# Kernel tuning notes

Measured on AMD Instinct MI355X. Metric: run time of the kernel, lower is better.

The kernel has to match this reference:

```python
import jax, jax.numpy as jnp
import numpy as np
import math

B, S, L, K, NSTEPS = 32, 128, 4096, 129, 10
PAD = K // 2  # torch: int(kernel.shape[-1]/2)


def _grouped_xcorr(x, w):
    # torch F.conv1d semantics (cross-correlation), groups = channels
    # x: [B,C,L] f32, w: [C,1,K] f32 -> [B,C,L]
    return jax.lax.conv_general_dilated(
        x, w, window_strides=(1,), padding=[(PAD, PAD)],
        dimension_numbers=('NCH', 'OIH', 'NCH'), feature_group_count=x.shape[1])


def _matched_filter(x_re, x_im, k_re, k_im):
    # complex grouped conv with conj(kernel) repeated per pulse
    wc_re = jnp.tile(k_re[None, None, :], (S, 1, 1))
    wc_im = jnp.tile(-k_im[None, None, :], (S, 1, 1))  # conj
    out_re = _grouped_xcorr(x_re, wc_re) - _grouped_xcorr(x_im, wc_im)
    out_im = _grouped_xcorr(x_re, wc_im) + _grouped_xcorr(x_im, wc_re)
    return out_re + 1j * out_im  # complex64 [B,S,L]


def _produce_rd(x, w_mag, w_phase):
    phase = jnp.arctan(w_phase)                    # [B,S]
    norm_mag = S * jax.nn.softmax(w_mag, axis=-1)  # [B,S]
    iq = (norm_mag * jnp.exp(-1j * phase))[..., None] * x
    return jnp.fft.fftshift(jnp.fft.fft(iq, axis=-2), axes=-2)


def _circular_weighted_mean(w):
    # circular weighted mean of index over last axis; returns (magnitude, index)
    N = w.shape[-1]
    ang = (2.0 * jnp.pi / N) * jnp.arange(N, dtype=w.dtype)
    z = jnp.sum(w * jnp.exp(1j * ang), axis=-1)
    return jnp.abs(z), jnp.angle(z) / (2.0 * jnp.pi) * N


def _snr(rd):
    Bn, nfft, Ln = rd.shape
    e = jnp.abs(rd) ** 2                                   # [B,S,L]
    flat_idx = jnp.argmax(e.reshape(Bn, -1), axis=1)
    max_range = flat_idx % Ln                              # [B] (indices: constant wrt grad)
    col = jnp.take_along_axis(e, max_range[:, None, None], axis=2)[..., 0]  # [B,S]
    _, peak_idx = _circular_weighted_mean(col)
    # torch rounds + casts to int -> detached index
    idx = jax.lax.stop_gradient(jnp.round(peak_idx)).astype(jnp.int32) % nfft
    peak = jnp.take_along_axis(col, idx[:, None], axis=1)[:, 0]
    noise = (jnp.sum(col, axis=-1) - peak) / (nfft - 1)
    return 10.0 * jnp.log10(peak) - 10.0 * jnp.log10(noise)


def setup_inputs() -> dict:
    key = jax.random.key(0)
    ks = jax.random.split(key, 5)
    return {
        'x_re': jax.random.normal(ks[0], (B, S, L), jnp.float32),
        'x_im': jax.random.normal(ks[1], (B, S, L), jnp.float32),
        'kernel_re': jax.random.normal(ks[2], (K,), jnp.float32),
        'kernel_im': jax.random.normal(ks[3], (K,), jnp.float32),
        'log_step_mag': -2.0 * jnp.ones((S, NSTEPS), jnp.float32),
        'log_step_phase': -2.0 * jnp.ones((S, NSTEPS), jnp.float32),
        'w_phase_init': jax.random.uniform(ks[4], (B, S), jnp.float32),
    }


def reference(x_re, x_im, kernel_re, kernel_im, log_step_mag, log_step_phase, w_phase_init):
    x = _matched_filter(x_re, x_im, kernel_re, kernel_im)  # [B,S,L] complex64
    w_mag = jnp.ones((B, S), jnp.float32)
    w_phase = w_phase_init

    def loss_sum(wm, wp):
        return jnp.sum(_snr(_produce_rd(x, wm, wp)))

    grad_fn = jax.grad(loss_sum, argnums=(0, 1))
    ln10 = math.log(10.0)
    for i in range(NSTEPS):
        # torch detaches w_mag/w_phase before the inner autograd.grad
        g_mag, g_phase = grad_fn(jax.lax.stop_gradient(w_mag),
                                 jax.lax.stop_gradient(w_phase))
        lr_mag = jnp.exp(log_step_mag[:, i] * ln10)    # 10**log_step
        lr_phase = jnp.exp(log_step_phase[:, i] * ln10)
        w_mag = w_mag + lr_mag * g_mag
        w_phase = w_phase + lr_phase * g_phase
    return jnp.mean(_snr(_produce_rd(x, w_mag, w_phase)))
```

## Files before the change

### kernel.cpp

```cpp
#include <hip/hip_runtime.h>

#define BB 32
#define SS 128
#define LL 4096
#define KK 129
#define NST 10

constexpr double PI_D = 3.141592653589793238462643383279502884;
constexpr double red_sin(double x){
  double x2 = x*x, t = x, r = x;
  t *= -x2/6.0;   r += t;
  t *= -x2/20.0;  r += t;
  t *= -x2/42.0;  r += t;
  t *= -x2/72.0;  r += t;
  t *= -x2/110.0; r += t;
  t *= -x2/156.0; r += t;
  t *= -x2/210.0; r += t;
  t *= -x2/272.0; r += t;
  return r;
}
constexpr double csin_d(double x){
  while (x >  PI_D) x -= 2.0*PI_D;
  while (x < -PI_D) x += 2.0*PI_D;
  if (x >  PI_D*0.5)      x =  PI_D - x;
  else if (x < -PI_D*0.5) x = -PI_D - x;
  return red_sin(x);
}
constexpr double ccos_d(double x){ return csin_d(x + PI_D*0.5); }
struct TWT { float c[64]; float s[64]; };
constexpr TWT make_tw(){
  TWT t{};
  for (int j = 0; j < 64; j++){
    double a = -2.0*PI_D*(double)j/128.0;
    t.c[j] = (float)ccos_d(a);
    t.s[j] = (float)csin_d(a);
  }
  return t;
}
constexpr TWT TW = make_tw();

__global__ __launch_bounds__(256) void mf_kernel(const float* __restrict__ xr,
                                                 const float* __restrict__ xi,
                                                 const float* __restrict__ kr,
                                                 const float* __restrict__ ki,
                                                 float2* __restrict__ out)
{
  const int row = blockIdx.x;
  const int t = threadIdx.x;
  __shared__ float2 xs[LL + KK - 1];
  __shared__ float2 ks[KK];
  const float* xrr = xr + (size_t)row*LL;
  const float* xir = xi + (size_t)row*LL;
  for (int i = t; i < LL + KK - 1; i += 256){
    int l = i - 64;
    float a = (l >= 0 && l < LL) ? xrr[l] : 0.0f;
    float c = (l >= 0 && l < LL) ? xir[l] : 0.0f;
    xs[i] = make_float2(a, c);
  }
  if (t < KK) ks[t] = make_float2(kr[t], ki[t]);
  __syncthreads();

  float2 acc[16];
  #pragma unroll
  for (int j = 0; j < 16; j++) acc[j] = make_float2(0.0f, 0.0f);

  for (int k = 0; k < KK; k++){
    const float2 w = ks[k];
    #pragma unroll
    for (int j = 0; j < 16; j++){
      float2 xv = xs[t + j*256 + k];
      acc[j].x += xv.x*w.x + xv.y*w.y;
      acc[j].y += xv.y*w.x - xv.x*w.y;
    }
  }
  float2* orow = out + (size_t)row*LL;
  #pragma unroll
  for (int j = 0; j < 16; j++) orow[t + j*256] = acc[j];
}

__global__ void init_kernel(const float* __restrict__ wpi,
                            float* __restrict__ w_mag, float* __restrict__ w_phase,
                            float2* __restrict__ cvec, unsigned long long* __restrict__ slots,
                            float* __restrict__ out)
{
  const int i = blockIdx.x*256 + threadIdx.x;
  if (i < BB*SS){
    float wp = wpi[i];
    w_mag[i] = 1.0f;
    w_phase[i] = wp;
    float phi = atanf(wp);
    float s, c;
    sincosf(phi, &s, &c);
    cvec[i] = make_float2(c, -s);
  }
  if (i < BB) slots[i] = 0ull;
  if (i == 0) out[0] = 0.0f;
}

template<int SPAN>
__device__ __forceinline__ void fstage(float2* v){
  #pragma unroll
  for (int base = 0; base < 64; base += 2*SPAN){
    #pragma unroll
    for (int j = 0; j < SPAN; j++){
      const int i0 = base + j, i1 = base + j + SPAN;
      float ax = v[i0].x, ay = v[i0].y, bx = v[i1].x, by = v[i1].y;
      float sx = ax - bx, sy = ay - by;
      v[i0].x = ax + bx; v[i0].y = ay + by;
      const int tj = j * (64 / SPAN);
      if (tj == 0){
        v[i1].x = sx; v[i1].y = sy;
      } else if (tj == 32){
        v[i1].x = sy; v[i1].y = -sx;
      } else {
        const float wr = TW.c[tj], wi = TW.s[tj];
        v[i1].x = sx*wr - sy*wi;
        v[i1].y = sy*wr + sx*wi;
      }
    }
  }
}

__global__ __launch_bounds__(256) void scan_kernel(const float2* __restrict__ xmf,
                                                   const float2* __restrict__ cvec,
                                                   unsigned long long* __restrict__ slots)
{
  const int b = blockIdx.y;
  const int tid = threadIdx.x;
  const int p = tid >> 1, r = tid & 1;
  const int l = blockIdx.x*128 + p;
  __shared__ float2 csh[SS];
  __shared__ unsigned long long red[256];
  if (tid < SS) csh[tid] = cvec[b*SS + tid];
  __syncthreads();

  const float2* xb = xmf + ((size_t)(b*SS + r*64))*LL + l;
  float2 v[64];
  #pragma unroll
  for (int j = 0; j < 64; j++){
    float2 x = xb[(size_t)j*LL];
    float2 c = csh[r*64 + j];
    v[j].x = c.x*x.x - c.y*x.y;
    v[j].y = c.x*x.y + c.y*x.x;
  }
  const float sgn = r ? -1.0f : 1.0f;
  #pragma unroll
  for (int j = 0; j < 64; j++){
    float px = __shfl_xor(v[j].x, 1);
    float py = __shfl_xor(v[j].y, 1);
    float ux = fmaf(sgn, v[j].x, px);
    float uy = fmaf(sgn, v[j].y, py);
    float wr = r ? TW.c[j] : 1.0f;
    float wi = r ? TW.s[j] : 0.0f;
    v[j].x = ux*wr - uy*wi;
    v[j].y = uy*wr + ux*wi;
  }
  fstage<32>(v); fstage<16>(v); fstage<8>(v);
  fstage<4>(v);  fstage<2>(v);  fstage<1>(v);

  float mm = 0.0f;
  #pragma unroll
  for (int j = 0; j < 64; j++) mm = fmaxf(mm, v[j].x*v[j].x + v[j].y*v[j].y);
  mm = fmaxf(mm, __shfl_xor(mm, 1));

  unsigned long long pk = ((unsigned long long)__float_as_uint(mm) << 32) | (unsigned int)l;
  red[tid] = pk;
  __syncthreads();
  #pragma unroll
  for (int st = 128; st > 0; st >>= 1){
    if (tid < st){ unsigned long long o = red[tid + st]; if (o > red[tid]) red[tid] = o; }
    __syncthreads();
  }
  if (tid == 0) atomicMax(slots + b, red[0]);
}

__device__ __forceinline__ float bsum(float v, float* red, int t){
  __syncthreads();
  red[t] = v; __syncthreads();
  #pragma unroll
  for (int st = 64; st > 0; st >>= 1){
    if (t < st) red[t] += red[t + st];
    __syncthreads();
  }
  return red[0];
}
__device__ __forceinline__ float bmax(float v, float* red, int t){
  __syncthreads();
  red[t] = v; __syncthreads();
  #pragma unroll
  for (int st = 64; st > 0; st >>= 1){
    if (t < st) red[t] = fmaxf(red[t], red[t + st]);
    __syncthreads();
  }
  return red[0];
}

__global__ __launch_bounds__(128) void step_kernel(const float2* __restrict__ xmf,
                                                   float* __restrict__ w_mag,
                                                   float* __restrict__ w_phase,
                                                   float2* __restrict__ cvec,
                                                   unsigned long long* __restrict__ slots,
                                                   const float* __restrict__ lsm,
                                                   const float* __restrict__ lsp,
                                                   int stepi, int isFinal,
                                                   float* __restrict__ out)
{
  const int b = blockIdx.x, t = threadIdx.x;
  __shared__ float red[128];
  __shared__ float2 ysh[128];
  __shared__ float twc[128], tws[128];
  __shared__ float speak;
  __shared__ int sidx;

  const int rbin = (int)(slots[b] & 0xffffffffull);
  float wm = w_mag[b*SS + t];
  float wp = w_phase[b*SS + t];
  const float2 xc = xmf[((size_t)(b*SS + t))*LL + rbin];
  float phi = atanf(wp);
  float sph, cph;
  sincosf(phi, &sph, &cph);
  {
    float sv, cv;
    sincosf((float)(2.0*PI_D/128.0) * (float)t, &sv, &cv);
    twc[t] = cv; tws[t] = -sv;
  }
  float mx = bmax(wm, red, t);
  float ex = expf(wm - mx);
  float sm = bsum(ex, red, t);
  float m = 128.0f * ex / sm;
  float cre = m*cph, cim = -m*sph;
  ysh[t] = make_float2(cre*xc.x - cim*xc.y, cre*xc.y + cim*xc.x);
  __syncthreads();

  float Fr = 0.0f, Fi = 0.0f;
  #pragma unroll 8
  for (int s2 = 0; s2 < 128; s2++){
    int id = (t*s2) & 127;
    float wr = twc[id], wi = tws[id];
    float2 ys = ysh[s2];
    Fr += wr*ys.x - wi*ys.y;
    Fi += wr*ys.y + wi*ys.x;
  }
  const int u = (t + 64) & 127;
  float colu = Fr*Fr + Fi*Fi;

  float total = bsum(colu, red, t);
  float zre = bsum(colu * twc[u], red, t);
  float zim = bsum(colu * (-tws[u]), red, t);
  if (t == 0){
    float ang = atan2f(zim, zre);
    float pidx = ang * (128.0f/(2.0f*(float)PI_D));
    float rr = rintf(pidx);
    sidx = ((int)rr) & 127;
  }
  __syncthreads();
  const int idx = sidx;
  if (u == idx) speak = colu;
  __syncthreads();
  const float peak = speak;
  const float noise = (total - peak) * (1.0f/127.0f);

  if (isFinal){
    if (t == 0) atomicAdd(out, 10.0f*(log10f(peak) - log10f(noise)) * (1.0f/(float)BB));
    return;
  }

  constexpr float C10 = 4.342944819032518f;
  float g = (u == idx) ? (C10/peak) : (-C10/(127.0f*noise));
  __syncthreads();
  ysh[t] = make_float2(2.0f*g*Fr, 2.0f*g*Fi);
  __syncthreads();

  float Tr = 0.0f, Ti = 0.0f;
  #pragma unroll 8
  for (int k = 0; k < 128; k++){
    int id = (t*k) & 127;
    float wr = twc[id], wi = -tws[id];
    float2 G = ysh[k];
    Tr += wr*G.x - wi*G.y;
    Ti += wr*G.y + wi*G.x;
  }
  float Hr = xc.x*Tr + xc.y*Ti;
  float Hi = xc.x*Ti - xc.y*Tr;
  float dm   = Hr*cph - Hi*sph;
  float dphi = -m*(Hr*sph + Hi*cph);
  float S1 = bsum(m*dm, red, t);
  float gwm = m*(dm - S1*(1.0f/128.0f));
  float gwp = dphi / (1.0f + wp*wp);

  constexpr float LN10 = 2.302585092994046f;
  float lrm = expf(lsm[t*NST + stepi] * LN10);
  float lrp = expf(lsp[t*NST + stepi] * LN10);
  wm += lrm*gwm;
  wp += lrp*gwp;
  w_mag[b*SS + t] = wm;
  w_phase[b*SS + t] = wp;

  float mx2 = bmax(wm, red, t);
  float ex2 = expf(wm - mx2);
  float sm2 = bsum(ex2, red, t);
  float m2 = 128.0f * ex2 / sm2;
  float phi2 = atanf(wp);
  float s2v, c2v;
  sincosf(phi2, &s2v, &c2v);
  cvec[b*SS + t] = make_float2(m2*c2v, -m2*s2v);
  if (t == 0) slots[b] = 0ull;
}

extern "C" void kernel_launch(void* const* d_in, const int* in_sizes, int n_in,
                              void* d_out, int out_size, void* d_ws, size_t ws_size,
                              hipStream_t stream)
{
  const float* x_re = (const float*)d_in[0];
  const float* x_im = (const float*)d_in[1];
  const float* k_re = (const float*)d_in[2];
  const float* k_im = (const float*)d_in[3];
  const float* lsm  = (const float*)d_in[4];
  const float* lsp  = (const float*)d_in[5];
  const float* wpi  = (const float*)d_in[6];
  float* out = (float*)d_out;

  char* ws = (char*)d_ws;
  size_t off = 0;
  float2* xmf = (float2*)(ws + off);                 off += (size_t)BB*SS*LL*sizeof(float2);
  unsigned long long* slots = (unsigned long long*)(ws + off); off += 256;
  float* w_mag   = (float*)(ws + off);               off += (size_t)BB*SS*4;
  float* w_phase = (float*)(ws + off);               off += (size_t)BB*SS*4;
  float2* cvec   = (float2*)(ws + off);              off += (size_t)BB*SS*8;
  if (ws_size < off) return;

  mf_kernel<<<BB*SS, 256, 0, stream>>>(x_re, x_im, k_re, k_im, xmf);
  init_kernel<<<(BB*SS + 255)/256, 256, 0, stream>>>(wpi, w_mag, w_phase, cvec, slots, out);
  for (int i = 0; i < NST; i++){
    scan_kernel<<<dim3(LL/128, BB), 256, 0, stream>>>(xmf, cvec, slots);
    step_kernel<<<BB, 128, 0, stream>>>(xmf, w_mag, w_phase, cvec, slots, lsm, lsp, i, 0, out);
  }
  scan_kernel<<<dim3(LL/128, BB), 256, 0, stream>>>(xmf, cvec, slots);
  step_kernel<<<BB, 128, 0, stream>>>(xmf, w_mag, w_phase, cvec, slots, lsm, lsp, 0, 1, out);
}
```

Measured before the change: 917.8 us.

## Register-window matched filter, 4-way split FFT scan, wave-shuffle reductions in step kernel

```diff
diff --git a/kernel.cpp b/kernel.cpp
--- a/kernel.cpp
+++ b/kernel.cpp
@@ -39,6 +39,8 @@
 }
 constexpr TWT TW = make_tw();
 
+#define PHYS(i) ((i) + (((i) >> 4) << 1))
+
 __global__ __launch_bounds__(256) void mf_kernel(const float* __restrict__ xr,
                                                  const float* __restrict__ xi,
                                                  const float* __restrict__ kr,
@@ -47,7 +49,7 @@
 {
   const int row = blockIdx.x;
   const int t = threadIdx.x;
-  __shared__ float2 xs[LL + KK - 1];
+  __shared__ float2 xs[4752];
   __shared__ float2 ks[KK];
   const float* xrr = xr + (size_t)row*LL;
   const float* xir = xi + (size_t)row*LL;
@@ -55,27 +57,62 @@
     int l = i - 64;
     float a = (l >= 0 && l < LL) ? xrr[l] : 0.0f;
     float c = (l >= 0 && l < LL) ? xir[l] : 0.0f;
-    xs[i] = make_float2(a, c);
+    xs[PHYS(i)] = make_float2(a, c);
   }
   if (t < KK) ks[t] = make_float2(kr[t], ki[t]);
   __syncthreads();
 
+  const int base = t*16;
   float2 acc[16];
   #pragma unroll
   for (int j = 0; j < 16; j++) acc[j] = make_float2(0.0f, 0.0f);
 
-  for (int k = 0; k < KK; k++){
-    const float2 w = ks[k];
+  float2 win[32];
+  #pragma unroll
+  for (int i = 0; i < 32; i++) win[i] = xs[PHYS(base + i)];
+
+  #pragma unroll 1
+  for (int kb2 = 0; kb2 < 4; ++kb2){
     #pragma unroll
-    for (int j = 0; j < 16; j++){
-      float2 xv = xs[t + j*256 + k];
-      acc[j].x += xv.x*w.x + xv.y*w.y;
-      acc[j].y += xv.y*w.x - xv.x*w.y;
+    for (int half = 0; half < 2; ++half){
+      #pragma unroll
+      for (int kk = 0; kk < 16; ++kk){
+        const float2 w = ks[kb2*32 + half*16 + kk];
+        #pragma unroll
+        for (int j = 0; j < 16; ++j){
+          const float2 xv = win[(half*16 + kk + j) & 31];
+          acc[j].x = fmaf(xv.x, w.x, acc[j].x);
+          acc[j].x = fmaf(xv.y, w.y, acc[j].x);
+          acc[j].y = fmaf(xv.y, w.x, acc[j].y);
+          acc[j].y = fmaf(-xv.x, w.y, acc[j].y);
+        }
+      }
+      if (kb2 < 3 || half == 0){
+        const int vb = kb2*32 + half*16 + 32;
+        #pragma unroll
+        for (int i = 0; i < 16; ++i){
+          win[half*16 + i] = xs[PHYS(base + vb + i)];
+        }
+      }
     }
   }
-  float2* orow = out + (size_t)row*LL;
-  #pragma unroll
-  for (int j = 0; j < 16; j++) orow[t + j*256] = acc[j];
+  {
+    const float2 w = ks[128];
+    #pragma unroll
+    for (int j = 0; j < 16; ++j){
+      const float2 xv = win[j];
+      acc[j].x = fmaf(xv.x, w.x, acc[j].x);
+      acc[j].x = fmaf(xv.y, w.y, acc[j].x);
+      acc[j].y = fmaf(xv.y, w.x, acc[j].y);
+      acc[j].y = fmaf(-xv.x, w.y, acc[j].y);
+    }
+  }
+
+  float4* orow = (float4*)(out + (size_t)row*LL + base);
+  #pragma unroll
+  for (int q = 0; q < 8; ++q){
+    orow[q] = make_float4(acc[2*q].x, acc[2*q].y, acc[2*q+1].x, acc[2*q+1].y);
+  }
 }
 
 __global__ void init_kernel(const float* __restrict__ wpi,
@@ -97,13 +134,13 @@
   if (i == 0) out[0] = 0.0f;
 }
 
-template<int SPAN>
+template<int SPAN, int N>
 __device__ __forceinline__ void fstage(float2* v){
   #pragma unroll
-  for (int base = 0; base < 64; base += 2*SPAN){
+  for (int b0 = 0; b0 < N; b0 += 2*SPAN){
     #pragma unroll
     for (int j = 0; j < SPAN; j++){
-      const int i0 = base + j, i1 = base + j + SPAN;
+      const int i0 = b0 + j, i1 = b0 + j + SPAN;
       float ax = v[i0].x, ay = v[i0].y, bx = v[i1].x, by = v[i1].y;
       float sx = ax - bx, sy = ay - by;
       v[i0].x = ax + bx; v[i0].y = ay + by;
@@ -127,75 +164,95 @@
 {
   const int b = blockIdx.y;
   const int tid = threadIdx.x;
-  const int p = tid >> 1, r = tid & 1;
-  const int l = blockIdx.x*128 + p;
+  const int f = tid >> 2, r = tid & 3;
+  const int l = blockIdx.x*64 + f;
   __shared__ float2 csh[SS];
-  __shared__ unsigned long long red[256];
   if (tid < SS) csh[tid] = cvec[b*SS + tid];
   __syncthreads();
 
-  const float2* xb = xmf + ((size_t)(b*SS + r*64))*LL + l;
-  float2 v[64];
-  #pragma unroll
-  for (int j = 0; j < 64; j++){
+  const float2* xb = xmf + ((size_t)(b*SS + r*32))*LL + l;
+  float2 v[32];
+  #pragma unroll
+  for (int j = 0; j < 32; ++j){
     float2 x = xb[(size_t)j*LL];
-    float2 c = csh[r*64 + j];
+    float2 c = csh[r*32 + j];
     v[j].x = c.x*x.x - c.y*x.y;
     v[j].y = c.x*x.y + c.y*x.x;
   }
-  const float sgn = r ? -1.0f : 1.0f;
-  #pragma unroll
-  for (int j = 0; j < 64; j++){
-    float px = __shfl_xor(v[j].x, 1);
-    float py = __shfl_xor(v[j].y, 1);
-    float ux = fmaf(sgn, v[j].x, px);
-    float uy = fmaf(sgn, v[j].y, py);
-    float wr = r ? TW.c[j] : 1.0f;
-    float wi = r ? TW.s[j] : 0.0f;
-    v[j].x = ux*wr - uy*wi;
-    v[j].y = uy*wr + ux*wi;
-  }
-  fstage<32>(v); fstage<16>(v); fstage<8>(v);
-  fstage<4>(v);  fstage<2>(v);  fstage<1>(v);
+  {
+    const bool hi = (r & 2) != 0;
+    const float sgn = hi ? -1.0f : 1.0f;
+    const bool odd = (r & 1) != 0;
+    #pragma unroll
+    for (int j = 0; j < 32; ++j){
+      float px = __shfl_xor(v[j].x, 2);
+      float py = __shfl_xor(v[j].y, 2);
+      float ux = fmaf(sgn, v[j].x, px);
+      float uy = fmaf(sgn, v[j].y, py);
+      float wr = hi ? (odd ? TW.s[j] : TW.c[j]) : 1.0f;
+      float wi = hi ? (odd ? -TW.c[j] : TW.s[j]) : 0.0f;
+      v[j].x = ux*wr - uy*wi;
+      v[j].y = uy*wr + ux*wi;
+    }
+  }
+  {
+    const bool hi = (r & 1) != 0;
+    const float sgn = hi ? -1.0f : 1.0f;
+    #pragma unroll
+    for (int j = 0; j < 32; ++j){
+      float px = __shfl_xor(v[j].x, 1);
+      float py = __shfl_xor(v[j].y, 1);
+      float ux = fmaf(sgn, v[j].x, px);
+      float uy = fmaf(sgn, v[j].y, py);
+      float wr = hi ? TW.c[2*j] : 1.0f;
+      float wi = hi ? TW.s[2*j] : 0.0f;
+      v[j].x = ux*wr - uy*wi;
+      v[j].y = uy*wr + ux*wi;
+    }
+  }
+  fstage<16,32>(v); fstage<8,32>(v); fstage<4,32>(v); fstage<2,32>(v); fstage<1,32>(v);
 
   float mm = 0.0f;
   #pragma unroll
-  for (int j = 0; j < 64; j++) mm = fmaxf(mm, v[j].x*v[j].x + v[j].y*v[j].y);
+  for (int j = 0; j < 32; ++j) mm = fmaxf(mm, v[j].x*v[j].x + v[j].y*v[j].y);
   mm = fmaxf(mm, __shfl_xor(mm, 1));
+  mm = fmaxf(mm, __shfl_xor(mm, 2));
 
   unsigned long long pk = ((unsigned long long)__float_as_uint(mm) << 32) | (unsigned int)l;
-  red[tid] = pk;
-  __syncthreads();
-  #pragma unroll
-  for (int st = 128; st > 0; st >>= 1){
-    if (tid < st){ unsigned long long o = red[tid + st]; if (o > red[tid]) red[tid] = o; }
-    __syncthreads();
-  }
-  if (tid == 0) atomicMax(slots + b, red[0]);
-}
-
-__device__ __forceinline__ float bsum(float v, float* red, int t){
-  __syncthreads();
-  red[t] = v; __syncthreads();
-  #pragma unroll
-  for (int st = 64; st > 0; st >>= 1){
-    if (t < st) red[t] += red[t + st];
-    __syncthreads();
-  }
-  return red[0];
-}
-__device__ __forceinline__ float bmax(float v, float* red, int t){
-  __syncthreads();
-  red[t] = v; __syncthreads();
-  #pragma unroll
-  for (int st = 64; st > 0; st >>= 1){
-    if (t < st) red[t] = fmaxf(red[t], red[t + st]);
-    __syncthreads();
-  }
-  return red[0];
-}
-
-__global__ __launch_bounds__(128) void step_kernel(const float2* __restrict__ xmf,
+  #pragma unroll
+  for (int m = 4; m < 64; m <<= 1){
+    unsigned long long o = __shfl_xor(pk, m);
+    if (o > pk) pk = o;
+  }
+  if ((tid & 63) == 0) atomicMax(slots + b, pk);
+}
+
+__device__ __forceinline__ float wredsum(float v){
+  #pragma unroll
+  for (int m = 1; m < 64; m <<= 1) v += __shfl_xor(v, m);
+  return v;
+}
+__device__ __forceinline__ float wredmax(float v){
+  #pragma unroll
+  for (int m = 1; m < 64; m <<= 1) v = fmaxf(v, __shfl_xor(v, m));
+  return v;
+}
+__device__ __forceinline__ float bsum256(float v, float* red4, int t){
+  v = wredsum(v);
+  __syncthreads();
+  if ((t & 63) == 0) red4[t >> 6] = v;
+  __syncthreads();
+  return red4[0] + red4[1] + red4[2] + red4[3];
+}
+__device__ __forceinline__ float bmax256(float v, float* red4, int t){
+  v = wredmax(v);
+  __syncthreads();
+  if ((t & 63) == 0) red4[t >> 6] = v;
+  __syncthreads();
+  return fmaxf(fmaxf(red4[0], red4[1]), fmaxf(red4[2], red4[3]));
+}
+
+__global__ __launch_bounds__(256) void step_kernel(const float2* __restrict__ xmf,
                                                    float* __restrict__ w_mag,
                                                    float* __restrict__ w_phase,
                                                    float2* __restrict__ cvec,
@@ -206,56 +263,61 @@
                                                    float* __restrict__ out)
 {
   const int b = blockIdx.x, t = threadIdx.x;
-  __shared__ float red[128];
-  __shared__ float2 ysh[128];
-  __shared__ float twc[128], tws[128];
+  const int s = t >> 1, h = t & 1;
+  __shared__ float2 ysh[SS];
+  __shared__ float twc[SS], tws[SS];
+  __shared__ float red4[4];
   __shared__ float speak;
   __shared__ int sidx;
 
   const int rbin = (int)(slots[b] & 0xffffffffull);
-  float wm = w_mag[b*SS + t];
-  float wp = w_phase[b*SS + t];
-  const float2 xc = xmf[((size_t)(b*SS + t))*LL + rbin];
-  float phi = atanf(wp);
+  const float wm0 = w_mag[b*SS + s];
+  const float wp0 = w_phase[b*SS + s];
+  const float2 xc = xmf[((size_t)(b*SS + s))*LL + rbin];
+  float phi = atanf(wp0);
   float sph, cph;
   sincosf(phi, &sph, &cph);
   {
+    int id = t & 127;
     float sv, cv;
-    sincosf((float)(2.0*PI_D/128.0) * (float)t, &sv, &cv);
-    twc[t] = cv; tws[t] = -sv;
-  }
-  float mx = bmax(wm, red, t);
-  float ex = expf(wm - mx);
-  float sm = bsum(ex, red, t);
+    sincosf((float)(2.0*PI_D/128.0) * (float)id, &sv, &cv);
+    twc[id] = cv; tws[id] = -sv;
+  }
+  float mx = bmax256(wm0, red4, t);
+  float ex = expf(wm0 - mx);
+  float sm = bsum256(ex, red4, t) * 0.5f;
   float m = 128.0f * ex / sm;
   float cre = m*cph, cim = -m*sph;
-  ysh[t] = make_float2(cre*xc.x - cim*xc.y, cre*xc.y + cim*xc.x);
-  __syncthreads();
-
+  ysh[s] = make_float2(cre*xc.x - cim*xc.y, cre*xc.y + cim*xc.x);
+  __syncthreads();
+
+  const int k = s;
   float Fr = 0.0f, Fi = 0.0f;
   #pragma unroll 8
-  for (int s2 = 0; s2 < 128; s2++){
-    int id = (t*s2) & 127;
+  for (int q = 0; q < 64; ++q){
+    int s2 = h*64 + q;
+    int id = (k*s2) & 127;
     float wr = twc[id], wi = tws[id];
     float2 ys = ysh[s2];
     Fr += wr*ys.x - wi*ys.y;
     Fi += wr*ys.y + wi*ys.x;
   }
-  const int u = (t + 64) & 127;
+  Fr += __shfl_xor(Fr, 1);
+  Fi += __shfl_xor(Fi, 1);
+  const int u = (k + 64) & 127;
   float colu = Fr*Fr + Fi*Fi;
 
-  float total = bsum(colu, red, t);
-  float zre = bsum(colu * twc[u], red, t);
-  float zim = bsum(colu * (-tws[u]), red, t);
+  float total = bsum256(colu, red4, t) * 0.5f;
+  float zre = bsum256(colu * twc[u], red4, t) * 0.5f;
+  float zim = bsum256(colu * (-tws[u]), red4, t) * 0.5f;
   if (t == 0){
     float ang = atan2f(zim, zre);
     float pidx = ang * (128.0f/(2.0f*(float)PI_D));
-    float rr = rintf(pidx);
-    sidx = ((int)rr) & 127;
+    sidx = ((int)rintf(pidx)) & 127;
   }
   __syncthreads();
   const int idx = sidx;
-  if (u == idx) speak = colu;
+  if (u == idx && h == 0) speak = colu;
   __syncthreads();
   const float peak = speak;
   const float noise = (total - peak) * (1.0f/127.0f);
@@ -268,42 +330,48 @@
   constexpr float C10 = 4.342944819032518f;
   float g = (u == idx) ? (C10/peak) : (-C10/(127.0f*noise));
   __syncthreads();
-  ysh[t] = make_float2(2.0f*g*Fr, 2.0f*g*Fi);
+  ysh[k] = make_float2(2.0f*g*Fr, 2.0f*g*Fi);
   __syncthreads();
 
   float Tr = 0.0f, Ti = 0.0f;
   #pragma unroll 8
-  for (int k = 0; k < 128; k++){
-    int id = (t*k) & 127;
+  for (int q = 0; q < 64; ++q){
+    int kk = h*64 + q;
+    int id = (s*kk) & 127;
     float wr = twc[id], wi = -tws[id];
-    float2 G = ysh[k];
+    float2 G = ysh[kk];
     Tr += wr*G.x - wi*G.y;
     Ti += wr*G.y + wi*G.x;
   }
+  Tr += __shfl_xor(Tr, 1);
+  Ti += __shfl_xor(Ti, 1);
+
   float Hr = xc.x*Tr + xc.y*Ti;
   float Hi = xc.x*Ti - xc.y*Tr;
   float dm   = Hr*cph - Hi*sph;
   float dphi = -m*(Hr*sph + Hi*cph);
-  float S1 = bsum(m*dm, red, t);
+  float S1 = bsum256(m*dm, red4, t) * 0.5f;
   float gwm = m*(dm - S1*(1.0f/128.0f));
-  float gwp = dphi / (1.0f + wp*wp);
+  float gwp = dphi / (1.0f + wp0*wp0);
 
   constexpr float LN10 = 2.302585092994046f;
-  float lrm = expf(lsm[t*NST + stepi] * LN10);
-  float lrp = expf(lsp[t*NST + stepi] * LN10);
-  wm += lrm*gwm;
-  wp += lrp*gwp;
-  w_mag[b*SS + t] = wm;
-  w_phase[b*SS + t] = wp;
-
-  float mx2 = bmax(wm, red, t);
-  float ex2 = expf(wm - mx2);
-  float sm2 = bsum(ex2, red, t);
+  float lrm = expf(lsm[s*NST + stepi] * LN10);
+  float lrp = expf(lsp[s*NST + stepi] * LN10);
+  float wm1 = wm0 + lrm*gwm;
+  float wp1 = wp0 + lrp*gwp;
+  if (h == 0){
+    w_mag[b*SS + s] = wm1;
+    w_phase[b*SS + s] = wp1;
+  }
+
+  float mx2 = bmax256(wm1, red4, t);
+  float ex2 = expf(wm1 - mx2);
+  float sm2 = bsum256(ex2, red4, t) * 0.5f;
   float m2 = 128.0f * ex2 / sm2;
-  float phi2 = atanf(wp);
+  float phi2 = atanf(wp1);
   float s2v, c2v;
   sincosf(phi2, &s2v, &c2v);
-  cvec[b*SS + t] = make_float2(m2*c2v, -m2*s2v);
+  if (h == 0) cvec[b*SS + s] = make_float2(m2*c2v, -m2*s2v);
   if (t == 0) slots[b] = 0ull;
 }
 
@@ -332,9 +400,9 @@
   mf_kernel<<<BB*SS, 256, 0, stream>>>(x_re, x_im, k_re, k_im, xmf);
   init_kernel<<<(BB*SS + 255)/256, 256, 0, stream>>>(wpi, w_mag, w_phase, cvec, slots, out);
   for (int i = 0; i < NST; i++){
-    scan_kernel<<<dim3(LL/128, BB), 256, 0, stream>>>(xmf, cvec, slots);
-    step_kernel<<<BB, 128, 0, stream>>>(xmf, w_mag, w_phase, cvec, slots, lsm, lsp, i, 0, out);
-  }
-  scan_kernel<<<dim3(LL/128, BB), 256, 0, stream>>>(xmf, cvec, slots);
-  step_kernel<<<BB, 128, 0, stream>>>(xmf, w_mag, w_phase, cvec, slots, lsm, lsp, 0, 1, out);
-}
+    scan_kernel<<<dim3(LL/64, BB), 256, 0, stream>>>(xmf, cvec, slots);
+    step_kernel<<<BB, 256, 0, stream>>>(xmf, w_mag, w_phase, cvec, slots, lsm, lsp, i, 0, out);
+  }
+  scan_kernel<<<dim3(LL/64, BB), 256, 0, stream>>>(xmf, cvec, slots);
+  step_kernel<<<BB, 256, 0, stream>>>(xmf, w_mag, w_phase, cvec, slots, lsm, lsp, 0, 1, out);
+}
```

Result: slower. 1.172 ms (+27.7%).
